# Optimization experiments

Hardware: AMD Instinct MI355X
Metric: run time of the kernel (lower is better)

The kernel has to match this reference:

```python
import jax, jax.numpy as jnp
import numpy as np

N = 100000
E = 3200000
HOP = 10

def setup_inputs() -> dict:
    key = jax.random.key(0)
    ks = jax.random.split(key, 10)
    n_in, n_hid, n_out = 512, 256, 64
    x = jax.random.normal(ks[0], (N, n_in), dtype=jnp.float32)
    edge_row = jax.random.randint(ks[1], (E,), 0, N, dtype=jnp.int32)
    edge_col = jax.random.randint(ks[2], (E,), 0, N, dtype=jnp.int32)
    # row-normalized-ish positive edge values (like a transition matrix)
    edge_vals = jax.random.uniform(ks[3], (E,), dtype=jnp.float32) / 32.0
    A2 = jax.random.uniform(ks[4], (N, 1), dtype=jnp.float32)
    # xavier-ish init scaled down for numerical sanity
    W1 = jax.random.normal(ks[5], (n_in, n_hid), dtype=jnp.float32) * (2.0 / (n_in + n_hid)) ** 0.5
    b1 = jnp.zeros((n_hid,), dtype=jnp.float32)
    W3 = jax.random.normal(ks[6], (n_hid, n_hid), dtype=jnp.float32) * (2.0 / (2 * n_hid)) ** 0.5
    b3 = jnp.zeros((n_hid,), dtype=jnp.float32)
    W2 = jax.random.normal(ks[7], (n_hid, n_out), dtype=jnp.float32) * (2.0 / (n_hid + n_out)) ** 0.5
    b2 = jnp.zeros((n_out,), dtype=jnp.float32)
    return {"x": x, "edge_row": edge_row, "edge_col": edge_col, "edge_vals": edge_vals,
            "A2": A2, "W1": W1, "b1": b1, "W3": W3, "b3": b3, "W2": W2, "b2": b2}

def _spmm(edge_row, edge_col, edge_vals, h):
    # sparse [N,N] @ dense [N,F] via gather + segment_sum
    msgs = edge_vals[:, None] * h[edge_col]          # [E, F]
    return jax.ops.segment_sum(msgs, edge_row, num_segments=N)

def reference(x, edge_row, edge_col, edge_vals, A2, W1, b1, W3, b3, W2, b2):
    # dropout layers are identity at eval time
    x0 = jax.nn.relu(x @ W1 + b1)                    # [N, n_hid]
    h = x0
    for _ in range(HOP):
        h = _spmm(edge_row, edge_col, edge_vals, h) + A2 * x0
        h = jax.nn.relu(h + h @ W3 + b3)
    return h @ W2 + b2                               # [N, n_out]
```

## Files before the change

kernel.cpp:

```cpp
#include <hip/hip_runtime.h>
#include <stdint.h>


typedef unsigned short bf16_t;
typedef __attribute__((ext_vector_type(8))) short bf16x8;
typedef __attribute__((ext_vector_type(8))) unsigned short u16x8;
typedef __attribute__((ext_vector_type(4))) float f32x4;

__device__ __forceinline__ float bf2f(bf16_t u) {
    union { unsigned int i; float f; } v; v.i = ((unsigned int)u) << 16; return v.f;
}
__device__ __forceinline__ bf16_t f2bf(float f) {
    union { float f; unsigned int i; } v; v.f = f;
    unsigned int x = v.i;
    unsigned int r = (x + 0x7fffu + ((x >> 16) & 1u)) >> 16;
    return (bf16_t)r;
}

__global__ void zero_i32(int* __restrict__ p, int n) {
    int i = blockIdx.x * blockDim.x + threadIdx.x;
    if (i < n) p[i] = 0;
}

__global__ void transpose_w(const float* __restrict__ W, bf16_t* __restrict__ Wt,
                            int K, int N) {
    int i = blockIdx.x * blockDim.x + threadIdx.x;
    if (i < K * N) {
        int k = i / N, n = i % N;
        Wt[(size_t)n * K + k] = f2bf(W[i]);
    }
}

__global__ void count_edges(const int* __restrict__ er, int* __restrict__ cnt,
                            int E, int N) {
    int i = blockIdx.x * blockDim.x + threadIdx.x;
    if (i < E) {
        unsigned r = (unsigned)er[i];
        if (r < (unsigned)N) atomicAdd(&cnt[r], 1);
    }
}

__global__ __launch_bounds__(1024)
void scan_rows(int* cnt_cursor, int* __restrict__ row_ptr, int n) {
    __shared__ int sums[1024];
    int t = threadIdx.x;
    int chunk = (n + 1023) >> 10;
    int start = t * chunk;
    int end = min(start + chunk, n);
    int s = 0;
    for (int i = start; i < end; ++i) s += cnt_cursor[i];
    sums[t] = s;
    __syncthreads();
    for (int off = 1; off < 1024; off <<= 1) {
        int v = (t >= off) ? sums[t - off] : 0;
        __syncthreads();
        sums[t] += v;
        __syncthreads();
    }
    int run = (t == 0) ? 0 : sums[t - 1];
    for (int i = start; i < end; ++i) {
        int c = cnt_cursor[i];
        row_ptr[i] = run;
        run += c;
    }
    if (t == 1023) row_ptr[n] = sums[1023];
}

__global__ void init_bcur(const int* __restrict__ row_ptr, int* __restrict__ bcur,
                          int N, int NB) {
    int b = blockIdx.x * blockDim.x + threadIdx.x;
    if (b < NB) bcur[b] = row_ptr[min(b << 8, N)];
}

#define BIN_CHUNK 8192
#define NBMAX 392
__global__ __launch_bounds__(256)
void bin_edges(const int* __restrict__ er, const int* __restrict__ ec,
               const float* __restrict__ ev, int* __restrict__ bcur,
               int2* __restrict__ binned, int E, int N, int NB) {
    __shared__ int cnt[NBMAX];
    __shared__ int resv[NBMAX];
    int tid = threadIdx.x;
    int e0 = blockIdx.x * BIN_CHUNK;
    int n = min(BIN_CHUNK, E - e0);
    for (int b = tid; b < NB; b += 256) cnt[b] = 0;
    __syncthreads();
    for (int i = tid; i < n; i += 256) {
        unsigned r = (unsigned)er[e0 + i];
        if (r < (unsigned)N) atomicAdd(&cnt[r >> 8], 1);
    }
    __syncthreads();
    for (int b = tid; b < NB; b += 256) {
        int c = cnt[b];
        resv[b] = c ? atomicAdd(&bcur[b], c) : 0;
        cnt[b] = 0;
    }
    __syncthreads();
    for (int i = tid; i < n; i += 256) {
        unsigned r = (unsigned)er[e0 + i];
        if (r < (unsigned)N) {
            unsigned c = (unsigned)ec[e0 + i];
            float v = ev[e0 + i];
            if (c >= (unsigned)N) { c = 0; v = 0.f; }
            int b = (int)(r >> 8);
            int p = resv[b] + atomicAdd(&cnt[b], 1);
            binned[p] = make_int2((int)(((r & 255u) << 17) | c), __float_as_int(v));
        }
    }
}

#define BCAP 9216
__global__ __launch_bounds__(256)
void bucket_sort(const int* __restrict__ row_ptr, int2* __restrict__ csr, int N) {
    __shared__ int2 ent[BCAP];
    __shared__ int cnt[256];
    __shared__ int base[256];
    __shared__ int lcur[256];
    int b = blockIdx.x;
    int tid = threadIdx.x;
    int r0 = b << 8;
    int e0 = row_ptr[r0];
    int e1 = row_ptr[min(r0 + 256, N)];
    int n = e1 - e0;
    cnt[tid] = 0;
    __syncthreads();
    for (int i = tid; i < n; i += 256) {
        int2 p = csr[e0 + i];
        if (i < BCAP) ent[i] = p;
        atomicAdd(&cnt[((unsigned)p.x >> 17) & 255u], 1);
    }
    __syncthreads();
    int v0 = cnt[tid];
    for (int off = 1; off < 256; off <<= 1) {
        int u = (tid >= off) ? cnt[tid - off] : 0;
        __syncthreads();
        cnt[tid] += u;
        __syncthreads();
    }
    base[tid] = cnt[tid] - v0;
    lcur[tid] = 0;
    __syncthreads();
    for (int i = tid; i < n; i += 256) {
        int2 p = (i < BCAP) ? ent[i] : csr[e0 + i];
        int rl = (int)(((unsigned)p.x >> 17) & 255u);
        int d = base[rl] + atomicAdd(&lcur[rl], 1);
        csr[e0 + d] = make_int2(p.x & 0x1FFFF, p.y);
    }
}

__device__ __forceinline__ void fma8(float* acc, float v, u16x8 hv) {
    #pragma unroll
    for (int k = 0; k < 8; ++k)
        acc[k] = fmaf(v, bf2f((bf16_t)hv[k]), acc[k]);
}

__global__ __launch_bounds__(256)
void spmm_kernel(const int* __restrict__ row_ptr, const int2* __restrict__ csr,
                 const bf16_t* __restrict__ h, const bf16_t* __restrict__ x0,
                 const float* __restrict__ A2, bf16_t* __restrict__ s, int N) {
    int w = threadIdx.x >> 6;
    int lane = threadIdx.x & 63;
    int row = (blockIdx.x << 2) + w;
    if (row >= N) return;
    int half = lane >> 5;
    int l32 = lane & 31;
    int fo = l32 << 3;
    int base = (row << 8) + fo;

    float acc[8];
    if (half == 0) {
        float a2 = A2[row];
        u16x8 xv = *(const u16x8*)&x0[base];
        #pragma unroll
        for (int k = 0; k < 8; ++k) acc[k] = a2 * bf2f((bf16_t)xv[k]);
    } else {
        #pragma unroll
        for (int k = 0; k < 8; ++k) acc[k] = 0.f;
    }

    int e = row_ptr[row], e1 = row_ptr[row + 1];
    int nb = (e1 - e) >> 3;
    int2 q0, q1, q2, q3;
    if (nb > 0) {
        int eb = e + half;
        q0 = csr[eb]; q1 = csr[eb + 2]; q2 = csr[eb + 4]; q3 = csr[eb + 6];
    }
    for (int b = 0; b < nb; ++b) {
        int2 p0 = q0, p1 = q1, p2 = q2, p3 = q3;
        if (b + 1 < nb) {
            int eb = e + 8 + half;
            q0 = csr[eb]; q1 = csr[eb + 2]; q2 = csr[eb + 4]; q3 = csr[eb + 6];
        }
        u16x8 h0 = *(const u16x8*)&h[(p0.x << 8) + fo];
        u16x8 h1 = *(const u16x8*)&h[(p1.x << 8) + fo];
        u16x8 h2 = *(const u16x8*)&h[(p2.x << 8) + fo];
        u16x8 h3 = *(const u16x8*)&h[(p3.x << 8) + fo];
        fma8(acc, __int_as_float(p0.y), h0);
        fma8(acc, __int_as_float(p1.y), h1);
        fma8(acc, __int_as_float(p2.y), h2);
        fma8(acc, __int_as_float(p3.y), h3);
        e += 8;
    }
    for (; e + 2 <= e1; e += 2) {
        int2 p = csr[e + half];
        u16x8 hv = *(const u16x8*)&h[(p.x << 8) + fo];
        fma8(acc, __int_as_float(p.y), hv);
    }
    if (e < e1 && half == 0) {
        int2 p = csr[e];
        u16x8 hv = *(const u16x8*)&h[(p.x << 8) + fo];
        fma8(acc, __int_as_float(p.y), hv);
    }

    #pragma unroll
    for (int k = 0; k < 8; ++k) acc[k] += __shfl_xor(acc[k], 32, 64);
    if (half == 0) {
        u16x8 o;
        #pragma unroll
        for (int k = 0; k < 8; ++k) o[k] = f2bf(acc[k]);
        *(u16x8*)&s[base] = o;
    }
}

template <int WM, int WN, bool AF32, bool SKIP, bool RELU, typename CT>
__global__ __launch_bounds__(256)
void mfma_gemm(const void* __restrict__ Av, const bf16_t* __restrict__ Bt,
               const float* __restrict__ bias, CT* __restrict__ C,
               int M, int K, int Nfull) {
    constexpr int TM = WM * 64;
    constexpr int TN = WN * 64;
    __shared__ bf16_t As[TM * 32];
    __shared__ bf16_t Bs[TN * 32];
    const int tid = threadIdx.x;
    const int w = tid >> 6, lane = tid & 63;
    const int q = lane >> 4, l16 = lane & 15;
    const int bm = blockIdx.x * TM;
    const int bn = blockIdx.y * TN;
    const int wm = (w % WM) * 64;
    const int wn = (w / WM) * 64;

    f32x4 acc[4][4] = {};

    for (int k0 = 0; k0 < K; k0 += 32) {
        if constexpr (AF32) {
            const float* A = (const float*)Av;
            int row = tid >> 1;
            int gr = min(bm + row, M - 1);
            const float* src = A + (size_t)gr * K + k0 + (tid & 1) * 16;
            bf16_t* dst = As + row * 32 + (tid & 1) * 16;
            #pragma unroll
            for (int g = 0; g < 4; ++g) {
                float4 v = *(const float4*)(src + 4 * g);
                ushort4 u;
                u.x = f2bf(v.x); u.y = f2bf(v.y); u.z = f2bf(v.z); u.w = f2bf(v.w);
                *(ushort4*)(dst + 4 * g) = u;
            }
        } else {
            const bf16_t* A = (const bf16_t*)Av;
            #pragma unroll
            for (int r = 0; r < TM / 64; ++r) {
                int rowbase = r * 64 + w * 16;
                int row = rowbase + (lane >> 2);
                int gr = min(bm + row, M - 1);
                const bf16_t* gp = A + (size_t)gr * K + k0 + (lane & 3) * 8;
                bf16_t* lp = As + rowbase * 32 + lane * 8;
                __builtin_amdgcn_global_load_lds(
                    (const __attribute__((address_space(1))) unsigned int*)gp,
                    (__attribute__((address_space(3))) unsigned int*)lp, 16, 0, 0);
            }
        }
        #pragma unroll
        for (int r = 0; r < TN / 64; ++r) {
            int rowbase = r * 64 + w * 16;
            int row = rowbase + (lane >> 2);
            const bf16_t* gp = Bt + (size_t)(bn + row) * K + k0 + (lane & 3) * 8;
            bf16_t* lp = Bs + rowbase * 32 + lane * 8;
            __builtin_amdgcn_global_load_lds(
                (const __attribute__((address_space(1))) unsigned int*)gp,
                (__attribute__((address_space(3))) unsigned int*)lp, 16, 0, 0);
        }
        __syncthreads();

        bf16x8 afr[4], bfr[4];
        #pragma unroll
        for (int ms = 0; ms < 4; ++ms)
            afr[ms] = *(const bf16x8*)&As[(wm + ms * 16 + l16) * 32 + q * 8];
        #pragma unroll
        for (int ns = 0; ns < 4; ++ns)
            bfr[ns] = *(const bf16x8*)&Bs[(wn + ns * 16 + l16) * 32 + q * 8];
        #pragma unroll
        for (int ms = 0; ms < 4; ++ms)
            #pragma unroll
            for (int ns = 0; ns < 4; ++ns)
                acc[ms][ns] = __builtin_amdgcn_mfma_f32_16x16x32_bf16(
                    afr[ms], bfr[ns], acc[ms][ns], 0, 0, 0);
        __syncthreads();
    }

    const bf16_t* Askip = (const bf16_t*)Av;
    #pragma unroll
    for (int ms = 0; ms < 4; ++ms) {
        #pragma unroll
        for (int r = 0; r < 4; ++r) {
            int row = bm + wm + ms * 16 + q * 4 + r;
            if (row < M) {
                #pragma unroll
                for (int ns = 0; ns < 4; ++ns) {
                    int col = bn + wn + ns * 16 + l16;
                    float v = acc[ms][ns][r] + bias[col];
                    if constexpr (SKIP) v += bf2f(Askip[(size_t)row * K + col]);
                    if constexpr (RELU) v = fmaxf(v, 0.f);
                    if constexpr (sizeof(CT) == 2) C[(size_t)row * Nfull + col] = (CT)f2bf(v);
                    else                           C[(size_t)row * Nfull + col] = (CT)v;
                }
            }
        }
    }
}

extern "C" void kernel_launch(void* const* d_in, const int* in_sizes, int n_in,
                              void* d_out, int out_size, void* d_ws, size_t ws_size,
                              hipStream_t stream) {
    const float* x   = (const float*)d_in[0];
    const int* erow  = (const int*)d_in[1];
    const int* ecol  = (const int*)d_in[2];
    const float* ev  = (const float*)d_in[3];
    const float* A2  = (const float*)d_in[4];
    const float* W1  = (const float*)d_in[5];
    const float* b1  = (const float*)d_in[6];
    const float* W3  = (const float*)d_in[7];
    const float* b3  = (const float*)d_in[8];
    const float* W2  = (const float*)d_in[9];
    const float* b2  = (const float*)d_in[10];
    float* out = (float*)d_out;

    const int N   = in_sizes[4];
    const int E   = in_sizes[1];
    const int NIN = in_sizes[0] / N;
    const int NH  = in_sizes[6];
    const int NO  = in_sizes[10];
    if (NH != 256 || NIN != 512 || NO != 64) return;
    const int NB = (N + 255) >> 8;
    if (NB > NBMAX) return;

    char* ws = (char*)d_ws;
    size_t off = 0;
    auto alloc = [&](size_t bytes) -> void* {
        void* p = ws + off;
        off += (bytes + 255) & ~(size_t)255;
        return p;
    };
    bf16_t* x0     = (bf16_t*)alloc((size_t)N * NH * 2);
    bf16_t* hA     = (bf16_t*)alloc((size_t)N * NH * 2);
    bf16_t* hB     = (bf16_t*)alloc((size_t)N * NH * 2);
    int*   row_ptr = (int*)alloc((size_t)(N + 1) * 4);
    int*   counts  = (int*)alloc((size_t)N * 4);
    int*   bcur    = (int*)alloc((size_t)NB * 4);
    int2*  csr     = (int2*)alloc((size_t)E * 8);
    bf16_t* W1t    = (bf16_t*)alloc((size_t)NIN * NH * 2);
    bf16_t* W3t    = (bf16_t*)alloc((size_t)NH * NH * 2);
    bf16_t* W2t    = (bf16_t*)alloc((size_t)NH * NO * 2);
    if (off > ws_size) return;

    zero_i32<<<(N + 255) / 256, 256, 0, stream>>>(counts, N);
    count_edges<<<(E + 255) / 256, 256, 0, stream>>>(erow, counts, E, N);
    scan_rows<<<1, 1024, 0, stream>>>(counts, row_ptr, N);
    init_bcur<<<(NB + 255) / 256, 256, 0, stream>>>(row_ptr, bcur, N, NB);
    bin_edges<<<(E + BIN_CHUNK - 1) / BIN_CHUNK, 256, 0, stream>>>(
        erow, ecol, ev, bcur, csr, E, N, NB);
    bucket_sort<<<NB, 256, 0, stream>>>(row_ptr, csr, N);
    transpose_w<<<(NIN * NH + 255) / 256, 256, 0, stream>>>(W1, W1t, NIN, NH);
    transpose_w<<<(NH * NH + 255) / 256, 256, 0, stream>>>(W3, W3t, NH, NH);
    transpose_w<<<(NH * NO + 255) / 256, 256, 0, stream>>>(W2, W2t, NH, NO);

    dim3 g1((N + 127) / 128, NH / 128);
    mfma_gemm<2, 2, true, false, true, bf16_t><<<g1, 256, 0, stream>>>(
        x, W1t, b1, x0, N, NIN, NH);

    const bf16_t* hin = x0;
    for (int hop = 0; hop < 10; ++hop) {
        spmm_kernel<<<(N + 3) / 4, 256, 0, stream>>>(row_ptr, csr, hin, x0, A2, hB, N);
        mfma_gemm<2, 2, false, true, true, bf16_t><<<g1, 256, 0, stream>>>(
            hB, W3t, b3, hA, N, NH, NH);
        hin = hA;
    }

    dim3 g2((N + 255) / 256, 1);
    mfma_gemm<4, 1, false, false, false, float><<<g2, 256, 0, stream>>>(
        hA, W2t, b2, out, N, NH, NO);
}
```

Before: 3.457 ms.

## Fuse SpMM aggregation with W3 GEMM per 128-row tile in LDS

Each hop now runs a single kernel. A 512-thread block gathers 128 rows of the sparse aggregate into a swizzled 64KB LDS tile, then multiplies that tile by W3 with MFMA and applies the skip connection, bias and ReLU from LDS. This removes the round trip of the intermediate s matrix through global memory and one launch per hop. In exchange it uses more LDS per block, which lowers occupancy for the latency-bound gather phase, and the output buffers ping-pong. The first GEMM is also retiled to 64x256 so that one block covers every column of a row tile.

Measured after the change: 3.367 ms. 2.6% less time.

```diff
diff --git a/kernel.cpp b/kernel.cpp
--- a/kernel.cpp
+++ b/kernel.cpp
@@ -154,75 +154,132 @@
         acc[k] = fmaf(v, bf2f((bf16_t)hv[k]), acc[k]);
 }
 
-__global__ __launch_bounds__(256)
-void spmm_kernel(const int* __restrict__ row_ptr, const int2* __restrict__ csr,
-                 const bf16_t* __restrict__ h, const bf16_t* __restrict__ x0,
-                 const float* __restrict__ A2, bf16_t* __restrict__ s, int N) {
-    int w = threadIdx.x >> 6;
-    int lane = threadIdx.x & 63;
-    int row = (blockIdx.x << 2) + w;
-    if (row >= N) return;
-    int half = lane >> 5;
-    int l32 = lane & 31;
-    int fo = l32 << 3;
-    int base = (row << 8) + fo;
-
-    float acc[8];
-    if (half == 0) {
-        float a2 = A2[row];
-        u16x8 xv = *(const u16x8*)&x0[base];
-        #pragma unroll
-        for (int k = 0; k < 8; ++k) acc[k] = a2 * bf2f((bf16_t)xv[k]);
-    } else {
+__global__ __launch_bounds__(512, 4)
+void fused_hop(const int* __restrict__ row_ptr, const int2* __restrict__ csr,
+               const bf16_t* __restrict__ hin, const bf16_t* __restrict__ x0,
+               const float* __restrict__ A2, const bf16_t* __restrict__ W3t,
+               const float* __restrict__ bias, bf16_t* __restrict__ hout, int M) {
+    __shared__ bf16_t s_tile[128 * 256];
+    __shared__ bf16_t Bs[256 * 32];
+    const int tid = threadIdx.x;
+    const int w = tid >> 6, lane = tid & 63;
+    const int bm = blockIdx.x * 128;
+    const int half = lane >> 5, l32 = lane & 31, fo = l32 << 3;
+
+    for (int rr = 0; rr < 16; ++rr) {
+        int lrow = w * 16 + rr;
+        int row = bm + lrow;
+        float acc[8];
         #pragma unroll
         for (int k = 0; k < 8; ++k) acc[k] = 0.f;
-    }
-
-    int e = row_ptr[row], e1 = row_ptr[row + 1];
-    int nb = (e1 - e) >> 3;
-    int2 q0, q1, q2, q3;
-    if (nb > 0) {
-        int eb = e + half;
-        q0 = csr[eb]; q1 = csr[eb + 2]; q2 = csr[eb + 4]; q3 = csr[eb + 6];
-    }
-    for (int b = 0; b < nb; ++b) {
-        int2 p0 = q0, p1 = q1, p2 = q2, p3 = q3;
-        if (b + 1 < nb) {
-            int eb = e + 8 + half;
-            q0 = csr[eb]; q1 = csr[eb + 2]; q2 = csr[eb + 4]; q3 = csr[eb + 6];
-        }
-        u16x8 h0 = *(const u16x8*)&h[(p0.x << 8) + fo];
-        u16x8 h1 = *(const u16x8*)&h[(p1.x << 8) + fo];
-        u16x8 h2 = *(const u16x8*)&h[(p2.x << 8) + fo];
-        u16x8 h3 = *(const u16x8*)&h[(p3.x << 8) + fo];
-        fma8(acc, __int_as_float(p0.y), h0);
-        fma8(acc, __int_as_float(p1.y), h1);
-        fma8(acc, __int_as_float(p2.y), h2);
-        fma8(acc, __int_as_float(p3.y), h3);
-        e += 8;
-    }
-    for (; e + 2 <= e1; e += 2) {
-        int2 p = csr[e + half];
-        u16x8 hv = *(const u16x8*)&h[(p.x << 8) + fo];
-        fma8(acc, __int_as_float(p.y), hv);
-    }
-    if (e < e1 && half == 0) {
-        int2 p = csr[e];
-        u16x8 hv = *(const u16x8*)&h[(p.x << 8) + fo];
-        fma8(acc, __int_as_float(p.y), hv);
+        if (row < M) {
+            if (half == 0) {
+                float a2 = A2[row];
+                u16x8 xv = *(const u16x8*)&x0[(row << 8) + fo];
+                #pragma unroll
+                for (int k = 0; k < 8; ++k) acc[k] = a2 * bf2f((bf16_t)xv[k]);
+            }
+            int e = row_ptr[row], e1 = row_ptr[row + 1];
+            int nb = (e1 - e) >> 3;
+            int2 q0, q1, q2, q3;
+            if (nb > 0) {
+                int eb = e + half;
+                q0 = csr[eb]; q1 = csr[eb + 2]; q2 = csr[eb + 4]; q3 = csr[eb + 6];
+            }
+            for (int b = 0; b < nb; ++b) {
+                int2 p0 = q0, p1 = q1, p2 = q2, p3 = q3;
+                if (b + 1 < nb) {
+                    int eb = e + 8 + half;
+                    q0 = csr[eb]; q1 = csr[eb + 2]; q2 = csr[eb + 4]; q3 = csr[eb + 6];
+                }
+                u16x8 h0 = *(const u16x8*)&hin[(p0.x << 8) + fo];
+                u16x8 h1 = *(const u16x8*)&hin[(p1.x << 8) + fo];
+                u16x8 h2 = *(const u16x8*)&hin[(p2.x << 8) + fo];
+                u16x8 h3 = *(const u16x8*)&hin[(p3.x << 8) + fo];
+                fma8(acc, __int_as_float(p0.y), h0);
+                fma8(acc, __int_as_float(p1.y), h1);
+                fma8(acc, __int_as_float(p2.y), h2);
+                fma8(acc, __int_as_float(p3.y), h3);
+                e += 8;
+            }
+            for (; e + 2 <= e1; e += 2) {
+                int2 p = csr[e + half];
+                u16x8 hv = *(const u16x8*)&hin[(p.x << 8) + fo];
+                fma8(acc, __int_as_float(p.y), hv);
+            }
+            if (e < e1 && half == 0) {
+                int2 p = csr[e];
+                u16x8 hv = *(const u16x8*)&hin[(p.x << 8) + fo];
+                fma8(acc, __int_as_float(p.y), hv);
+            }
+            #pragma unroll
+            for (int k = 0; k < 8; ++k) acc[k] += __shfl_xor(acc[k], 32, 64);
+        }
+        if (half == 0) {
+            u16x8 o;
+            #pragma unroll
+            for (int k = 0; k < 8; ++k) o[k] = f2bf(acc[k]);
+            *(u16x8*)((char*)s_tile + lrow * 512 + (((fo << 1)) ^ ((lrow & 7) << 4))) = o;
+        }
+    }
+    __syncthreads();
+
+    const int q = lane >> 4, l16 = lane & 15;
+    const int wm = (w & 1) * 64, wn = (w >> 1) * 64;
+    f32x4 acc2[4][4] = {};
+    for (int k0 = 0; k0 < 256; k0 += 32) {
+        #pragma unroll
+        for (int r = 0; r < 2; ++r) {
+            int rowbase = r * 128 + w * 16;
+            int row = rowbase + (lane >> 2);
+            const bf16_t* gp = W3t + (size_t)row * 256 + k0 + (lane & 3) * 8;
+            bf16_t* lp = Bs + rowbase * 32 + lane * 8;
+            __builtin_amdgcn_global_load_lds(
+                (const __attribute__((address_space(1))) unsigned int*)gp,
+                (__attribute__((address_space(3))) unsigned int*)lp, 16, 0, 0);
+        }
+        __syncthreads();
+        bf16x8 afr[4], bfr[4];
+        #pragma unroll
+        for (int ms = 0; ms < 4; ++ms) {
+            int ar = wm + ms * 16 + l16;
+            afr[ms] = *(const bf16x8*)((const char*)s_tile + ar * 512 +
+                       ((((k0 + q * 8) << 1)) ^ ((ar & 7) << 4)));
+        }
+        #pragma unroll
+        for (int ns = 0; ns < 4; ++ns)
+            bfr[ns] = *(const bf16x8*)&Bs[(wn + ns * 16 + l16) * 32 + q * 8];
+        #pragma unroll
+        for (int ms = 0; ms < 4; ++ms)
+            #pragma unroll
+            for (int ns = 0; ns < 4; ++ns)
+                acc2[ms][ns] = __builtin_amdgcn_mfma_f32_16x16x32_bf16(
+                    afr[ms], bfr[ns], acc2[ms][ns], 0, 0, 0);
+        __syncthreads();
     }
 
     #pragma unroll
-    for (int k = 0; k < 8; ++k) acc[k] += __shfl_xor(acc[k], 32, 64);
-    if (half == 0) {
-        u16x8 o;
-        #pragma unroll
-        for (int k = 0; k < 8; ++k) o[k] = f2bf(acc[k]);
-        *(u16x8*)&s[base] = o;
-    }
-}
-
-template <int WM, int WN, bool AF32, bool SKIP, bool RELU, typename CT>
+    for (int ms = 0; ms < 4; ++ms) {
+        #pragma unroll
+        for (int r = 0; r < 4; ++r) {
+            int lrow = wm + ms * 16 + q * 4 + r;
+            int grow = bm + lrow;
+            if (grow < M) {
+                #pragma unroll
+                for (int ns = 0; ns < 4; ++ns) {
+                    int col = wn + ns * 16 + l16;
+                    float v = acc2[ms][ns][r] + bias[col];
+                    v += bf2f(*(const bf16_t*)((const char*)s_tile + lrow * 512 +
+                              (((col << 1)) ^ ((lrow & 7) << 4))));
+                    v = fmaxf(v, 0.f);
+                    hout[(size_t)grow * 256 + col] = f2bf(v);
+                }
+            }
+        }
+    }
+}
+
+template <int WM, int WN, bool AF32, bool RELU, typename CT>
 __global__ __launch_bounds__(256)
 void mfma_gemm(const void* __restrict__ Av, const bf16_t* __restrict__ Bt,
                const float* __restrict__ bias, CT* __restrict__ C,
@@ -243,13 +300,16 @@
 
     for (int k0 = 0; k0 < K; k0 += 32) {
         if constexpr (AF32) {
+            constexpr int TPR = 256 / TM;
+            constexpr int EPT = TM / 8;
             const float* A = (const float*)Av;
-            int row = tid >> 1;
+            int row = tid / TPR;
             int gr = min(bm + row, M - 1);
-            const float* src = A + (size_t)gr * K + k0 + (tid & 1) * 16;
-            bf16_t* dst = As + row * 32 + (tid & 1) * 16;
-            #pragma unroll
-            for (int g = 0; g < 4; ++g) {
+            int off = (tid % TPR) * EPT;
+            const float* src = A + (size_t)gr * K + k0 + off;
+            bf16_t* dst = As + row * 32 + off;
+            #pragma unroll
+            for (int g = 0; g < EPT / 4; ++g) {
                 float4 v = *(const float4*)(src + 4 * g);
                 ushort4 u;
                 u.x = f2bf(v.x); u.y = f2bf(v.y); u.z = f2bf(v.z); u.w = f2bf(v.w);
@@ -297,7 +357,6 @@
         __syncthreads();
     }
 
-    const bf16_t* Askip = (const bf16_t*)Av;
     #pragma unroll
     for (int ms = 0; ms < 4; ++ms) {
         #pragma unroll
@@ -308,7 +367,6 @@
                 for (int ns = 0; ns < 4; ++ns) {
                     int col = bn + wn + ns * 16 + l16;
                     float v = acc[ms][ns][r] + bias[col];
-                    if constexpr (SKIP) v += bf2f(Askip[(size_t)row * K + col]);
                     if constexpr (RELU) v = fmaxf(v, 0.f);
                     if constexpr (sizeof(CT) == 2) C[(size_t)row * Nfull + col] = (CT)f2bf(v);
                     else                           C[(size_t)row * Nfull + col] = (CT)v;
@@ -373,19 +431,20 @@
     transpose_w<<<(NH * NH + 255) / 256, 256, 0, stream>>>(W3, W3t, NH, NH);
     transpose_w<<<(NH * NO + 255) / 256, 256, 0, stream>>>(W2, W2t, NH, NO);
 
-    dim3 g1((N + 127) / 128, NH / 128);
-    mfma_gemm<2, 2, true, false, true, bf16_t><<<g1, 256, 0, stream>>>(
+    dim3 g1((N + 63) / 64, 1);
+    mfma_gemm<1, 4, true, true, bf16_t><<<g1, 256, 0, stream>>>(
         x, W1t, b1, x0, N, NIN, NH);
 
     const bf16_t* hin = x0;
+    bf16_t* hout = hA;
     for (int hop = 0; hop < 10; ++hop) {
-        spmm_kernel<<<(N + 3) / 4, 256, 0, stream>>>(row_ptr, csr, hin, x0, A2, hB, N);
-        mfma_gemm<2, 2, false, true, true, bf16_t><<<g1, 256, 0, stream>>>(
-            hB, W3t, b3, hA, N, NH, NH);
-        hin = hA;
+        fused_hop<<<(N + 127) / 128, 512, 0, stream>>>(
+            row_ptr, csr, hin, x0, A2, W3t, b3, hout, N);
+        hin = hout;
+        hout = (hout == hA) ? hB : hA;
     }
 
     dim3 g2((N + 255) / 256, 1);
-    mfma_gemm<4, 1, false, false, false, float><<<g2, 256, 0, stream>>>(
-        hA, W2t, b2, out, N, NH, NO);
-}
+    mfma_gemm<4, 1, false, false, float><<<g2, 256, 0, stream>>>(
+        (const void*)hin, W2t, b2, out, N, NH, NO);
+}
```
